# Performance work log

Hardware: AMD Instinct MI355X
Metric: run time of the kernel (lower is better)

The kernel has to match this reference:

```python
import jax, jax.numpy as jnp
import numpy as np

OUT, IN, GROUP = 4096, 4096, 128
NG = IN // GROUP  # 32 groups along in_features
TOKENS = 8192

def setup_inputs() -> dict:
    key = jax.random.key(0)
    k1, k2, k3, k4, k5 = jax.random.split(key, 5)
    input = jax.random.normal(k1, (TOKENS, IN), dtype=jnp.float32)
    qweight = jax.random.randint(k2, (OUT, IN), 0, 16, dtype=jnp.int32)
    scales = jax.random.uniform(k3, (OUT, NG), dtype=jnp.float32) * 0.02 + 0.001
    zeros = jax.random.uniform(k4, (OUT, NG), dtype=jnp.float32) * 15.0
    bias = jax.random.normal(k5, (OUT,), dtype=jnp.float32)
    return {"input": input, "qweight": qweight, "scales": scales, "zeros": zeros, "bias": bias}

def dequantize(qweight, scales, zeros):
    # qweight: [OUT, IN] int; scales/zeros: [OUT, NG]; group along in_features
    q = qweight.astype(jnp.float32).reshape(OUT, NG, GROUP)
    w = (q - zeros[:, :, None]) * scales[:, :, None]
    return w.reshape(OUT, IN)

def reference(input, qweight, scales, zeros, bias):
    # F.linear(input, W, bias) == input @ W.T + bias
    W = dequantize(qweight, scales, zeros)
    return jnp.einsum('ti,oi->to', input, W) + bias
```

## Files before the change

kernel.cpp:

```cpp
#include <hip/hip_runtime.h>
#include <hip/hip_bf16.h>
#include <cstdint>

typedef __attribute__((ext_vector_type(4))) float  floatx4;
typedef __attribute__((ext_vector_type(8))) __bf16 bf16x8;

#define M_T 8192
#define N_T 4096
#define K_T 4096
#define NG  32

__device__ __forceinline__ unsigned short f2bf(float f) {
    union { float f; unsigned int u; } v; v.f = f;
    unsigned int u = v.u;
    u += 0x7fffu + ((u >> 16) & 1u);
    return (unsigned short)(u >> 16);
}

__device__ __forceinline__ void load_lds16(const void* gsrc, void* ldst) {
    __builtin_amdgcn_global_load_lds(
        (const __attribute__((address_space(1))) uint32_t*)gsrc,
        (__attribute__((address_space(3))) uint32_t*)ldst,
        16, 0, 0);
}

__global__ void dequant_w_kernel(const int* __restrict__ q,
                                 const float* __restrict__ sc,
                                 const float* __restrict__ zr,
                                 unsigned short* __restrict__ Wb) {
    int idx = blockIdx.x * 256 + threadIdx.x;
    int e0 = idx << 2;
    int row = e0 >> 12;
    int col = e0 & 4095;
    int g = col >> 7;
    float s = sc[(row << 5) + g];
    float z = zr[(row << 5) + g];
    int4 qv = *(const int4*)(q + e0);
    ushort4 o;
    o.x = f2bf(((float)qv.x - z) * s);
    o.y = f2bf(((float)qv.y - z) * s);
    o.z = f2bf(((float)qv.z - z) * s);
    o.w = f2bf(((float)qv.w - z) * s);
    *(ushort4*)(Wb + e0) = o;
}

__global__ void convert_x_kernel(const float* __restrict__ X,
                                 unsigned short* __restrict__ Xb) {
    int idx = blockIdx.x * 256 + threadIdx.x;
    int e0 = idx << 2;
    float4 xv = *(const float4*)(X + e0);
    ushort4 o;
    o.x = f2bf(xv.x); o.y = f2bf(xv.y); o.z = f2bf(xv.z); o.w = f2bf(xv.w);
    *(ushort4*)(Xb + e0) = o;
}

__global__ __launch_bounds__(512, 2) void gemm256_8ph(
    const unsigned short* __restrict__ Xb,
    const unsigned short* __restrict__ Wb,
    const float* __restrict__ bias,
    float* __restrict__ C)
{
    __shared__ __align__(16) unsigned short lds[65536];
    char* ldsb = (char*)lds;

    const int tid  = threadIdx.x;
    const int lane = tid & 63;
    const int wid  = tid >> 6;
    const int wm   = wid >> 2;
    const int wn   = wid & 3;

    int bid = blockIdx.x;
    int swz = (bid & 7) * 64 + (bid >> 3);
    const int bm = (swz & 31) * 256;
    const int bn = (swz >> 5) * 256;

    floatx4 acc[8][4] = {};

    const int klb = (lane >> 4) * 16;

    auto stage_half = [&](int buf, int isB, int half, int grow0, int k0,
                          const unsigned short* __restrict__ G) {
        char* base = ldsb + buf * 65536 + isB * 32768 + half * 16384;
        #pragma unroll
        for (int c = 0; c < 2; ++c) {
            int r  = c * 64 + wid * 8 + (lane >> 3);
            int cb = ((lane & 7) * 16) ^ ((lane >> 3) << 4);
            const char* src = (const char*)(G + (size_t)(grow0 + r) * K_T + k0) + cb;
            load_lds16(src, base + c * 8192 + wid * 1024);
        }
    };
    auto rdA = [&](int buf, int mf, int kb) -> bf16x8 {
        int r = mf * 16 + (lane & 15);
        int off = buf * 65536 + wm * 16384 + r * 128 + (kb ^ ((r & 7) << 4));
        return *(const bf16x8*)(ldsb + off);
    };
    auto rdB = [&](int buf, int nf, int kb) -> bf16x8 {
        int r = (wn & 1) * 64 + nf * 16 + (lane & 15);
        int off = buf * 65536 + 32768 + (wn >> 1) * 16384 + r * 128 + (kb ^ ((r & 7) << 4));
        return *(const bf16x8*)(ldsb + off);
    };

    stage_half(0, 1, 0, bn,       0,  Wb);
    stage_half(0, 1, 1, bn + 128, 0,  Wb);
    stage_half(0, 0, 0, bm,       0,  Xb);
    stage_half(0, 0, 1, bm + 128, 0,  Xb);
    stage_half(1, 1, 0, bn,       64, Wb);
    stage_half(1, 1, 1, bn + 128, 64, Wb);
    asm volatile("s_waitcnt vmcnt(4)" ::: "memory");
    asm volatile("" ::: "memory");
    __builtin_amdgcn_s_barrier();
    asm volatile("" ::: "memory");

    bf16x8 bfr[4][2];

    for (int t = 0; t < 32; ++t) {
        const int t1 = 2 * t + 1;
        const int t2 = (2 * t + 2 < 64) ? 2 * t + 2 : 63;
        const int t3 = (2 * t + 3 < 64) ? 2 * t + 3 : 63;
        #pragma unroll
        for (int p = 0; p < 8; ++p) {
            const int cb = p >> 2;
            const int q  = p & 3;

            if (q == 0) {
                #pragma unroll
                for (int nf = 0; nf < 4; ++nf)
                    #pragma unroll
                    for (int kk = 0; kk < 2; ++kk)
                        bfr[nf][kk] = rdB(cb, nf, kk * 64 + klb);
            }
            bf16x8 a[2][2];
            #pragma unroll
            for (int i = 0; i < 2; ++i)
                #pragma unroll
                for (int kk = 0; kk < 2; ++kk)
                    a[i][kk] = rdA(cb, 2 * q + i, kk * 64 + klb);

            switch (p) {
                case 0: stage_half(1, 0, 0, bm,       t1 * 64, Xb); break;
                case 1: stage_half(1, 0, 1, bm + 128, t1 * 64, Xb); break;
                case 2: stage_half(0, 1, 0, bn,       t2 * 64, Wb); break;
                case 3: stage_half(0, 1, 1, bn + 128, t2 * 64, Wb); break;
                case 4: stage_half(0, 0, 0, bm,       t2 * 64, Xb); break;
                case 5: stage_half(0, 0, 1, bm + 128, t2 * 64, Xb); break;
                case 6: stage_half(1, 1, 0, bn,       t3 * 64, Wb); break;
                case 7: stage_half(1, 1, 1, bn + 128, t3 * 64, Wb); break;
            }

            asm volatile("" ::: "memory");
            __builtin_amdgcn_s_barrier();
            asm volatile("" ::: "memory");

            __builtin_amdgcn_s_setprio(1);
            #pragma unroll
            for (int i = 0; i < 2; ++i)
                #pragma unroll
                for (int nf = 0; nf < 4; ++nf)
                    #pragma unroll
                    for (int kk = 0; kk < 2; ++kk)
                        acc[2 * q + i][nf] = __builtin_amdgcn_mfma_f32_16x16x32_bf16(
                            a[i][kk], bfr[nf][kk], acc[2 * q + i][nf], 0, 0, 0);
            __builtin_amdgcn_s_setprio(0);

            if (q == 3)
                asm volatile("s_waitcnt vmcnt(4)" ::: "memory");
            asm volatile("" ::: "memory");
            __builtin_amdgcn_s_barrier();
            asm volatile("" ::: "memory");
        }
    }

    asm volatile("s_waitcnt vmcnt(0)" ::: "memory");

    #pragma unroll
    for (int nf = 0; nf < 4; ++nf) {
        int col = bn + wn * 64 + nf * 16 + (lane & 15);
        float bv = bias[col];
        #pragma unroll
        for (int mf = 0; mf < 8; ++mf) {
            int row0 = bm + wm * 128 + mf * 16 + (lane >> 4) * 4;
            #pragma unroll
            for (int j = 0; j < 4; ++j)
                C[(size_t)(row0 + j) * N_T + col] = acc[mf][nf][j] + bv;
        }
    }
}

__global__ void fallback_gemm(const float* __restrict__ X,
                              const int* __restrict__ q,
                              const float* __restrict__ sc,
                              const float* __restrict__ zr,
                              const float* __restrict__ bias,
                              float* __restrict__ C) {
    __shared__ float sX[16][17];
    __shared__ float sW[16][17];
    int tx = threadIdx.x, ty = threadIdx.y;
    int row = blockIdx.y * 16 + ty;
    int col = blockIdx.x * 16 + tx;
    float acc = 0.f;
    for (int k0 = 0; k0 < K_T; k0 += 16) {
        sX[ty][tx] = X[(size_t)row * K_T + k0 + tx];
        int wrow = blockIdx.x * 16 + ty;
        int kc = k0 + tx;
        int g = kc >> 7;
        sW[ty][tx] = ((float)q[(size_t)wrow * K_T + kc] - zr[wrow * NG + g]) * sc[wrow * NG + g];
        __syncthreads();
        #pragma unroll
        for (int kk = 0; kk < 16; ++kk) acc += sX[ty][kk] * sW[tx][kk];
        __syncthreads();
    }
    C[(size_t)row * N_T + col] = acc + bias[col];
}

extern "C" void kernel_launch(void* const* d_in, const int* in_sizes, int n_in,
                              void* d_out, int out_size, void* d_ws, size_t ws_size,
                              hipStream_t stream) {
    const float* input   = (const float*)d_in[0];
    const int*   qweight = (const int*)d_in[1];
    const float* scales  = (const float*)d_in[2];
    const float* zeros   = (const float*)d_in[3];
    const float* bias    = (const float*)d_in[4];
    float* out = (float*)d_out;

    const size_t needW = (size_t)N_T * K_T * sizeof(unsigned short);
    const size_t needX = (size_t)M_T * K_T * sizeof(unsigned short);

    if (ws_size >= needW + needX) {
        unsigned short* Wb = (unsigned short*)d_ws;
        unsigned short* Xb = (unsigned short*)((char*)d_ws + needW);

        dequant_w_kernel<<<(N_T * K_T / 4) / 256, 256, 0, stream>>>(qweight, scales, zeros, Wb);
        convert_x_kernel<<<(M_T * K_T / 4) / 256, 256, 0, stream>>>(input, Xb);

        gemm256_8ph<<<512, 512, 0, stream>>>(Xb, Wb, bias, out);
    } else {
        dim3 blk(16, 16);
        dim3 grid(N_T / 16, M_T / 16);
        fallback_gemm<<<grid, blk, 0, stream>>>(input, qweight, scales, zeros, bias, out);
    }
}
```

Baseline: 320.9 us.

## Remap tiles per XCD for L2 locality and reorder MFMA phase k-split

Replaces the block swizzle so each XCD covers a compact 8x8 region of output tiles (4 M-groups by 2 N-groups), which should improve L2 reuse of X and W rows within each chiplet. Reorganizes the 4 phases per buffer so each phase handles 4 M fragments at a single k-half instead of 2 M fragments at both k-halves, loading the second B k-half at phase 1 and adding an lgkmcnt wait there. Some compiler memory fences around barriers are removed. The risk is changed register pressure and LDS read scheduling, and possible reordering hazards without the fences.

```diff
diff --git a/kernel.cpp b/kernel.cpp
--- a/kernel.cpp
+++ b/kernel.cpp
@@ -70,9 +70,11 @@
     const int wn   = wid & 3;
 
     int bid = blockIdx.x;
-    int swz = (bid & 7) * 64 + (bid >> 3);
-    const int bm = (swz & 31) * 256;
-    const int bn = (swz >> 5) * 256;
+    int xcd = bid & 7, r0 = bid >> 3;
+    int mt = (xcd >> 1) * 8 + (r0 & 7);
+    int nt = (xcd & 1) * 8 + (r0 >> 3);
+    const int bm = mt * 256;
+    const int bn = nt * 256;
 
     floatx4 acc[8][4] = {};
 
@@ -107,9 +109,7 @@
     stage_half(1, 1, 0, bn,       64, Wb);
     stage_half(1, 1, 1, bn + 128, 64, Wb);
     asm volatile("s_waitcnt vmcnt(4)" ::: "memory");
-    asm volatile("" ::: "memory");
     __builtin_amdgcn_s_barrier();
-    asm volatile("" ::: "memory");
 
     bf16x8 bfr[4][2];
 
@@ -119,22 +119,25 @@
         const int t3 = (2 * t + 3 < 64) ? 2 * t + 3 : 63;
         #pragma unroll
         for (int p = 0; p < 8; ++p) {
-            const int cb = p >> 2;
-            const int q  = p & 3;
+            const int cb    = p >> 2;
+            const int q     = p & 3;
+            const int mbase = (q & 1) * 4;
+            const int kkp   = q >> 1;
 
             if (q == 0) {
                 #pragma unroll
                 for (int nf = 0; nf < 4; ++nf)
-                    #pragma unroll
-                    for (int kk = 0; kk < 2; ++kk)
-                        bfr[nf][kk] = rdB(cb, nf, kk * 64 + klb);
+                    bfr[nf][0] = rdB(cb, nf, klb);
             }
-            bf16x8 a[2][2];
+            if (q == 1) {
+                #pragma unroll
+                for (int nf = 0; nf < 4; ++nf)
+                    bfr[nf][1] = rdB(cb, nf, 64 + klb);
+            }
+            bf16x8 a[4];
             #pragma unroll
-            for (int i = 0; i < 2; ++i)
-                #pragma unroll
-                for (int kk = 0; kk < 2; ++kk)
-                    a[i][kk] = rdA(cb, 2 * q + i, kk * 64 + klb);
+            for (int m = 0; m < 4; ++m)
+                a[m] = rdA(cb, mbase + m, kkp * 64 + klb);
 
             switch (p) {
                 case 0: stage_half(1, 0, 0, bm,       t1 * 64, Xb); break;
@@ -147,26 +150,22 @@
                 case 7: stage_half(1, 1, 1, bn + 128, t3 * 64, Wb); break;
             }
 
-            asm volatile("" ::: "memory");
             __builtin_amdgcn_s_barrier();
-            asm volatile("" ::: "memory");
 
             __builtin_amdgcn_s_setprio(1);
             #pragma unroll
-            for (int i = 0; i < 2; ++i)
+            for (int m = 0; m < 4; ++m)
                 #pragma unroll
                 for (int nf = 0; nf < 4; ++nf)
-                    #pragma unroll
-                    for (int kk = 0; kk < 2; ++kk)
-                        acc[2 * q + i][nf] = __builtin_amdgcn_mfma_f32_16x16x32_bf16(
-                            a[i][kk], bfr[nf][kk], acc[2 * q + i][nf], 0, 0, 0);
+                    acc[mbase + m][nf] = __builtin_amdgcn_mfma_f32_16x16x32_bf16(
+                        a[m], bfr[nf][kkp], acc[mbase + m][nf], 0, 0, 0);
             __builtin_amdgcn_s_setprio(0);
 
+            if (q == 1)
+                asm volatile("s_waitcnt lgkmcnt(0)" ::: "memory");
             if (q == 3)
                 asm volatile("s_waitcnt vmcnt(4)" ::: "memory");
-            asm volatile("" ::: "memory");
             __builtin_amdgcn_s_barrier();
-            asm volatile("" ::: "memory");
         }
     }
 
```

New measurement: 284.9 us. -11.2%, faster.
